# Kernel tuning notes

Hardware: AMD Instinct MI355X
Metric: run time of the kernel (lower is better)

Reference implementation:

```python
import jax, jax.numpy as jnp
import numpy as np

T, N, E, P, D, F = 24, 10000, 320000, 20000, 64, 32


def setup_inputs() -> dict:
    key = jax.random.key(0)
    ks = jax.random.split(key, 16)
    s = 0.05

    def nrm(k, shape):
        return jax.random.normal(k, shape, jnp.float32) * s

    return {
        "x": jax.random.normal(ks[0], (T, N, F + 2), jnp.float32),
        "dis": jax.random.uniform(ks[1], (N, N), dtype=jnp.float32),
        "src": jax.random.randint(ks[2], (E,), 0, N, jnp.int32),
        "dst": jax.random.randint(ks[3], (E,), 0, N, jnp.int32),
        "train_idx": jax.random.randint(ks[4], (2, P), 0, N, jnp.int32),
        "ru_W1": nrm(ks[5], (D + F, D)), "ru_b1": jnp.zeros((D,), jnp.float32),
        "ru_W2": nrm(ks[6], (D, D)), "ru_b2": jnp.zeros((D,), jnp.float32),
        "ru_W3": nrm(ks[7], (D, 2 * D)), "ru_b3": jnp.zeros((2 * D,), jnp.float32),
        "rh_W1": nrm(ks[8], (D + F, D)), "rh_b1": jnp.zeros((D,), jnp.float32),
        "rh_W2": nrm(ks[9], (D, D)), "rh_b2": jnp.zeros((D,), jnp.float32),
        "rh_W3": nrm(ks[10], (D, D)), "rh_b3": jnp.zeros((D,), jnp.float32),
        "pred_W": nrm(ks[11], (2 * D + 1, 1)), "pred_b": jnp.zeros((1,), jnp.float32),
    }


def reference(x, dis, src, dst, train_idx,
              ru_W1, ru_b1, ru_W2, ru_b2, ru_W3, ru_b3,
              rh_W1, rh_b1, rh_W2, rh_b2, rh_W3, rh_b3,
              pred_W, pred_b):
    # DGL GraphConv, norm='both': h <- D_in^{-1/2} A D_out^{-1/2} h W + b (deg clamped to >=1)
    ones = jnp.ones((E,), jnp.float32)
    out_norm = jax.lax.rsqrt(jnp.maximum(jax.ops.segment_sum(ones, src, num_segments=N), 1.0))
    in_norm = jax.lax.rsqrt(jnp.maximum(jax.ops.segment_sum(ones, dst, num_segments=N), 1.0))

    def gconv(h, W, b):
        m = (h * out_norm[:, None])[src]                              # gather [E, d]
        agg = jax.ops.segment_sum(m, dst, num_segments=N) * in_norm[:, None]
        return agg @ W + b

    def gnn(h, W1, b1, W2, b2, W3, b3):
        h = jax.nn.relu(gconv(h, W1, b1))
        h = jax.nn.relu(gconv(h, W2, b2))
        return gconv(h, W3, b3)

    feat = x[:, :, :-2]                                               # [T, N, F]

    def step(h, xt):
        ru = jax.nn.sigmoid(gnn(jnp.concatenate([h, xt], -1),
                                ru_W1, ru_b1, ru_W2, ru_b2, ru_W3, ru_b3))
        r, z = ru[:, :D], ru[:, D:]
        h_new = jnp.tanh(gnn(jnp.concatenate([h * r, xt], -1),
                             rh_W1, rh_b1, rh_W2, rh_b2, rh_W3, rh_b3))
        h = z * h + (1.0 - z) * h_new
        return h, h

    _, hs = jax.lax.scan(step, jnp.zeros((N, D), x.dtype), feat)      # [T, N, D]

    ori = hs[:, train_idx[0]]                                         # [T, P, D]
    dst_e = hs[:, train_idx[1]]                                       # [T, P, D]
    d = jnp.broadcast_to(dis[train_idx[0], train_idx[1]][None, :, None], (T, P, 1))
    flow = jnp.tanh(jnp.concatenate([ori, dst_e, d], -1) @ pred_W + pred_b)  # [T, P, 1]
    return flow[:, :, 0].T                                            # [P, T]
```

## Files before the change

### kernel.cpp

```cpp
#include <hip/hip_runtime.h>
#include <cstdint>
#include <cstddef>

#define T_ 24
#define N_ 10000
#define E_ 320000
#define P_ 20000
#define D_ 64
#define F_ 32
#define XS_ 34


__global__ void deg_kernel(const int* __restrict__ src, const int* __restrict__ dst,
                           int* __restrict__ deg_out, int* __restrict__ deg_in) {
  int e = blockIdx.x * blockDim.x + threadIdx.x;
  if (e < E_) {
    atomicAdd(&deg_out[src[e]], 1);
    atomicAdd(&deg_in[dst[e]], 1);
  }
}

__global__ void norm_kernel(const int* __restrict__ deg_in, const int* __restrict__ deg_out,
                            float* __restrict__ in_norm, float* __restrict__ out_norm) {
  int n = blockIdx.x * blockDim.x + threadIdx.x;
  if (n < N_) {
    in_norm[n]  = 1.0f / sqrtf(fmaxf((float)deg_in[n], 1.0f));
    out_norm[n] = 1.0f / sqrtf(fmaxf((float)deg_out[n], 1.0f));
  }
}

__global__ __launch_bounds__(1024) void scan_kernel(const int* __restrict__ deg,
                                                    int* __restrict__ row_ptr) {
  __shared__ int buf[1024];
  __shared__ int carry;
  int tid = threadIdx.x;
  if (tid == 0) { carry = 0; row_ptr[0] = 0; }
  __syncthreads();
  for (int base = 0; base < N_; base += 1024) {
    int i = base + tid;
    int v = (i < N_) ? deg[i] : 0;
    buf[tid] = v;
    __syncthreads();
    for (int off = 1; off < 1024; off <<= 1) {
      int tv = (tid >= off) ? buf[tid - off] : 0;
      __syncthreads();
      buf[tid] += tv;
      __syncthreads();
    }
    if (i < N_) row_ptr[i + 1] = carry + buf[tid];
    __syncthreads();
    if (tid == 0) carry += buf[1023];
    __syncthreads();
  }
}

__global__ void fill_kernel(const int* __restrict__ src, const int* __restrict__ dst,
                            const int* __restrict__ row_ptr, int* __restrict__ fill,
                            int* __restrict__ col) {
  int e = blockIdx.x * blockDim.x + threadIdx.x;
  if (e < E_) {
    int n = dst[e];
    int pos = row_ptr[n] + atomicAdd(&fill[n], 1);
    col[pos] = src[e];
  }
}

__global__ void dvec_kernel(const float* __restrict__ dis, const int* __restrict__ ti,
                            float* __restrict__ dvec) {
  int p = blockIdx.x * blockDim.x + threadIdx.x;
  if (p < P_) {
    int i0 = ti[p];
    int i1 = ti[P_ + p];
    dvec[p] = dis[(size_t)i0 * N_ + i1];
  }
}

__global__ __launch_bounds__(256) void pre_kernel(
    const float* __restrict__ hsrc, const float* __restrict__ xt,
    const float* __restrict__ out_norm, const float* __restrict__ W,
    float* __restrict__ tdst) {
  __shared__ float sIn[32][96];
  __shared__ float sW[96 * 64];
  const int tid = threadIdx.x;
  const int node0 = blockIdx.x * 32;

  {
    const float4* Wv = (const float4*)W;
    float4* sWv = (float4*)sW;
    for (int i = tid; i < 96 * 64 / 4; i += 256) sWv[i] = Wv[i];
  }
  for (int idx = tid; idx < 32 * 96; idx += 256) {
    int r = idx / 96, c = idx % 96;
    int n = node0 + r;
    float v = 0.0f;
    if (n < N_) {
      v = (c < 64) ? hsrc[(size_t)n * 64 + c] : xt[(size_t)n * XS_ + (c - 64)];
      v *= out_norm[n];
    }
    sIn[r][c] = v;
  }
  __syncthreads();

  const int o = tid & 63;
  const int q = tid >> 6;
  float acc[8];
#pragma unroll
  for (int j = 0; j < 8; ++j) acc[j] = 0.0f;
#pragma unroll 4
  for (int i = 0; i < 96; ++i) {
    float w = sW[i * 64 + o];
#pragma unroll
    for (int j = 0; j < 8; ++j) acc[j] += sIn[q * 8 + j][i] * w;
  }
#pragma unroll
  for (int j = 0; j < 8; ++j) {
    int n = node0 + q * 8 + j;
    if (n < N_) tdst[(size_t)n * 64 + o] = acc[j];
  }
}

template<int DOUT, int MODE>
__global__ __launch_bounds__(512) void gather_kernel(
    const float* __restrict__ t, const int* __restrict__ row_ptr,
    const int* __restrict__ col, const float* __restrict__ in_norm,
    const float* __restrict__ out_norm, const float* __restrict__ W,
    const float* __restrict__ bias, float* __restrict__ out,
    const float* __restrict__ hprev, float* __restrict__ hdst,
    const float* __restrict__ zsrc, float* __restrict__ zdst) {
  __shared__ float4 sAgg4[8][16];
  constexpr int WELEMS = (MODE == 1) ? 4 : (64 * DOUT);
  __shared__ float sW[WELEMS];

  const int tid = threadIdx.x;
  if constexpr (MODE != 1) {
    const float4* Wv = (const float4*)W;
    float4* sWv = (float4*)sW;
    for (int i = tid; i < WELEMS / 4; i += 512) sWv[i] = Wv[i];
  }

  const int wave = tid >> 6;
  const int lane = tid & 63;
  const int g = lane >> 4;
  const int sub = lane & 15;
  const int n = blockIdx.x * 8 + wave;

  float4 acc = make_float4(0.f, 0.f, 0.f, 0.f);
  if (n < N_) {
    int e0 = row_ptr[n], e1 = row_ptr[n + 1];
    int e = e0 + g;
    int snext = (e < e1) ? col[e] : 0;
    for (; e < e1; e += 4) {
      int s = snext;
      int en = e + 4;
      snext = (en < e1) ? col[en] : 0;
      float4 v = ((const float4*)(t + (size_t)s * 64))[sub];
      acc.x += v.x; acc.y += v.y; acc.z += v.z; acc.w += v.w;
    }
  }
#pragma unroll
  for (int off = 16; off < 64; off <<= 1) {
    acc.x += __shfl_xor(acc.x, off);
    acc.y += __shfl_xor(acc.y, off);
    acc.z += __shfl_xor(acc.z, off);
    acc.w += __shfl_xor(acc.w, off);
  }

  if (n < N_ && g == 0) {
    float inn = in_norm[n];
    float4 val;
    if constexpr (MODE == 0 || MODE == 1) {
      float on = out_norm[n];
      float4 b4 = ((const float4*)bias)[sub];
      val.x = on * fmaxf(inn * acc.x + b4.x, 0.0f);
      val.y = on * fmaxf(inn * acc.y + b4.y, 0.0f);
      val.z = on * fmaxf(inn * acc.z + b4.z, 0.0f);
      val.w = on * fmaxf(inn * acc.w + b4.w, 0.0f);
    } else {
      val.x = inn * acc.x; val.y = inn * acc.y;
      val.z = inn * acc.z; val.w = inn * acc.w;
    }
    if constexpr (MODE == 1) {
      ((float4*)(out + (size_t)n * 64))[sub] = val;
    } else {
      sAgg4[wave][sub] = val;
    }
  }
  if constexpr (MODE == 1) return;
  __syncthreads();

  if (n >= N_) return;
  const float* sAgg = (const float*)&sAgg4[wave][0];
  const int o = lane;

  if constexpr (MODE == 0) {
    float a = 0.0f;
#pragma unroll 8
    for (int i = 0; i < 64; ++i) a += sAgg[i] * sW[i * 64 + o];
    out[(size_t)n * 64 + o] = a;
  } else if constexpr (MODE == 2) {
    float a0 = bias[o], a1 = bias[o + 64];
#pragma unroll 8
    for (int i = 0; i < 64; ++i) {
      float ai = sAgg[i];
      a0 += ai * sW[i * 128 + o];
      a1 += ai * sW[i * 128 + o + 64];
    }
    float r = 1.0f / (1.0f + expf(-a0));
    float z = 1.0f / (1.0f + expf(-a1));
    hdst[(size_t)n * 64 + o] = r * hprev[(size_t)n * 64 + o];
    zdst[(size_t)n * 64 + o] = z;
  } else {
    float a = bias[o];
#pragma unroll 8
    for (int i = 0; i < 64; ++i) a += sAgg[i] * sW[i * 64 + o];
    float hn = tanhf(a);
    float zz = zsrc[(size_t)n * 64 + o];
    float hp = hprev[(size_t)n * 64 + o];
    hdst[(size_t)n * 64 + o] = zz * hp + (1.0f - zz) * hn;
  }
}

__global__ __launch_bounds__(256) void pred_kernel(
    const float* __restrict__ h, const int* __restrict__ ti,
    const float* __restrict__ dvec, const float* __restrict__ pW,
    const float* __restrict__ pb, float* __restrict__ out, int t) {
  const int tid = threadIdx.x;
  const int lane = tid & 63;
  const int wave = tid >> 6;
  const int g2 = lane >> 4;
  const int sub = lane & 15;
  const int p = blockIdx.x * 16 + wave * 4 + g2;
  if (p >= P_) return;

  int i0 = ti[p];
  int i1 = ti[P_ + p];
  float4 a0 = ((const float4*)(h + (size_t)i0 * 64))[sub];
  float4 w0 = ((const float4*)pW)[sub];
  float4 a1 = ((const float4*)(h + (size_t)i1 * 64))[sub];
  float4 w1 = ((const float4*)(pW + 64))[sub];
  float part = a0.x * w0.x + a0.y * w0.y + a0.z * w0.z + a0.w * w0.w
             + a1.x * w1.x + a1.y * w1.y + a1.z * w1.z + a1.w * w1.w;
#pragma unroll
  for (int off = 1; off < 16; off <<= 1) part += __shfl_xor(part, off);
  if (sub == 0) {
    float a = part + pb[0] + dvec[p] * pW[128];
    out[(size_t)p * T_ + t] = tanhf(a);
  }
}


extern "C" void kernel_launch(void* const* d_in, const int* in_sizes, int n_in,
                              void* d_out, int out_size, void* d_ws, size_t ws_size,
                              hipStream_t stream) {
  const float* x      = (const float*)d_in[0];
  const float* dis    = (const float*)d_in[1];
  const int*   src    = (const int*)d_in[2];
  const int*   dst    = (const int*)d_in[3];
  const int*   ti     = (const int*)d_in[4];
  const float* ru_W1  = (const float*)d_in[5];
  const float* ru_b1  = (const float*)d_in[6];
  const float* ru_W2  = (const float*)d_in[7];
  const float* ru_b2  = (const float*)d_in[8];
  const float* ru_W3  = (const float*)d_in[9];
  const float* ru_b3  = (const float*)d_in[10];
  const float* rh_W1  = (const float*)d_in[11];
  const float* rh_b1  = (const float*)d_in[12];
  const float* rh_W2  = (const float*)d_in[13];
  const float* rh_b2  = (const float*)d_in[14];
  const float* rh_W3  = (const float*)d_in[15];
  const float* rh_b3  = (const float*)d_in[16];
  const float* pred_W = (const float*)d_in[17];
  const float* pred_b = (const float*)d_in[18];
  float* out = (float*)d_out;

  char* w = (char*)d_ws;
  auto alloc = [&](size_t bytes) -> void* {
    void* p = (void*)w;
    w += (bytes + 255) & ~(size_t)255;
    return p;
  };
  int*   row_ptr  = (int*)alloc((N_ + 1) * sizeof(int));
  int*   colv     = (int*)alloc(E_ * sizeof(int));
  int*   deg_in   = (int*)alloc(N_ * sizeof(int));
  int*   deg_out  = (int*)alloc(N_ * sizeof(int));
  int*   fillc    = (int*)alloc(N_ * sizeof(int));
  float* in_norm  = (float*)alloc(N_ * sizeof(float));
  float* out_norm = (float*)alloc(N_ * sizeof(float));
  float* dvec     = (float*)alloc(P_ * sizeof(float));
  float* h        = (float*)alloc((size_t)N_ * D_ * sizeof(float));
  float* hr       = (float*)alloc((size_t)N_ * D_ * sizeof(float));
  float* z        = (float*)alloc((size_t)N_ * D_ * sizeof(float));
  float* tA       = (float*)alloc((size_t)N_ * D_ * sizeof(float));
  float* tB       = (float*)alloc((size_t)N_ * D_ * sizeof(float));

  hipMemsetAsync(deg_in, 0, N_ * sizeof(int), stream);
  hipMemsetAsync(deg_out, 0, N_ * sizeof(int), stream);
  hipMemsetAsync(fillc, 0, N_ * sizeof(int), stream);
  hipMemsetAsync(h, 0, (size_t)N_ * D_ * sizeof(float), stream);

  deg_kernel<<<(E_ + 255) / 256, 256, 0, stream>>>(src, dst, deg_out, deg_in);
  norm_kernel<<<(N_ + 255) / 256, 256, 0, stream>>>(deg_in, deg_out, in_norm, out_norm);
  scan_kernel<<<1, 1024, 0, stream>>>(deg_in, row_ptr);
  fill_kernel<<<(E_ + 255) / 256, 256, 0, stream>>>(src, dst, row_ptr, fillc, colv);
  dvec_kernel<<<(P_ + 255) / 256, 256, 0, stream>>>(dis, ti, dvec);

  const int GPRE = (N_ + 31) / 32;
  const int GGAT = (N_ + 7) / 8;
  const int GPRD = (P_ + 15) / 16;

  for (int t = 0; t < T_; ++t) {
    const float* xt = x + (size_t)t * N_ * XS_;
    pre_kernel<<<GPRE, 256, 0, stream>>>(h, xt, out_norm, ru_W1, tA);
    gather_kernel<64, 0><<<GGAT, 512, 0, stream>>>(
        tA, row_ptr, colv, in_norm, out_norm, ru_W2, ru_b1, tB,
        nullptr, nullptr, nullptr, nullptr);
    gather_kernel<64, 1><<<GGAT, 512, 0, stream>>>(
        tB, row_ptr, colv, in_norm, out_norm, nullptr, ru_b2, tA,
        nullptr, nullptr, nullptr, nullptr);
    gather_kernel<128, 2><<<GGAT, 512, 0, stream>>>(
        tA, row_ptr, colv, in_norm, out_norm, ru_W3, ru_b3, nullptr,
        h, hr, nullptr, z);
    pre_kernel<<<GPRE, 256, 0, stream>>>(hr, xt, out_norm, rh_W1, tA);
    gather_kernel<64, 0><<<GGAT, 512, 0, stream>>>(
        tA, row_ptr, colv, in_norm, out_norm, rh_W2, rh_b1, tB,
        nullptr, nullptr, nullptr, nullptr);
    gather_kernel<64, 1><<<GGAT, 512, 0, stream>>>(
        tB, row_ptr, colv, in_norm, out_norm, nullptr, rh_b2, tA,
        nullptr, nullptr, nullptr, nullptr);
    gather_kernel<64, 3><<<GGAT, 512, 0, stream>>>(
        tA, row_ptr, colv, in_norm, out_norm, rh_W3, rh_b3, nullptr,
        h, h, z, nullptr);
    pred_kernel<<<GPRD, 256, 0, stream>>>(h, ti, dvec, pred_W, pred_b, out, t);
  }
}
```

Measured before the change: 3.212 ms.

## Fuse all GRU timesteps into one persistent cooperative kernel with grid syncs

Replaces the 216 per-step kernel launches with a single cooperative persistent kernel that walks all timesteps and phases, separated by grid-wide barriers. The first-layer dense transform is folded into the preceding gather phase, so the hr buffer and the separate pre kernels go away. The prediction for step t-1 is run alongside the first phase of step t. The gather loop is also unrolled to keep two neighbour loads in flight. The aim is to remove launch gaps and intermediate memory round-trips, at the cost of 144 grid-wide barriers, a fixed grid size and possible load imbalance from contiguous node ranges.

```diff
diff --git a/kernel.cpp b/kernel.cpp
--- a/kernel.cpp
+++ b/kernel.cpp
@@ -1,4 +1,5 @@
 #include <hip/hip_runtime.h>
+#include <hip/hip_cooperative_groups.h>
 #include <cstdint>
 #include <cstddef>
 
@@ -9,6 +10,8 @@
 #define D_ 64
 #define F_ 32
 #define XS_ 34
+
+namespace cg = cooperative_groups;
 
 
 __global__ void deg_kernel(const int* __restrict__ src, const int* __restrict__ dst,
@@ -75,87 +78,50 @@
   }
 }
 
-__global__ __launch_bounds__(256) void pre_kernel(
-    const float* __restrict__ hsrc, const float* __restrict__ xt,
-    const float* __restrict__ out_norm, const float* __restrict__ W,
-    float* __restrict__ tdst) {
-  __shared__ float sIn[32][96];
-  __shared__ float sW[96 * 64];
-  const int tid = threadIdx.x;
-  const int node0 = blockIdx.x * 32;
-
-  {
-    const float4* Wv = (const float4*)W;
-    float4* sWv = (float4*)sW;
-    for (int i = tid; i < 96 * 64 / 4; i += 256) sWv[i] = Wv[i];
-  }
-  for (int idx = tid; idx < 32 * 96; idx += 256) {
-    int r = idx / 96, c = idx % 96;
-    int n = node0 + r;
-    float v = 0.0f;
-    if (n < N_) {
-      v = (c < 64) ? hsrc[(size_t)n * 64 + c] : xt[(size_t)n * XS_ + (c - 64)];
-      v *= out_norm[n];
-    }
-    sIn[r][c] = v;
-  }
-  __syncthreads();
-
-  const int o = tid & 63;
-  const int q = tid >> 6;
-  float acc[8];
-#pragma unroll
-  for (int j = 0; j < 8; ++j) acc[j] = 0.0f;
-#pragma unroll 4
-  for (int i = 0; i < 96; ++i) {
-    float w = sW[i * 64 + o];
-#pragma unroll
-    for (int j = 0; j < 8; ++j) acc[j] += sIn[q * 8 + j][i] * w;
-  }
-#pragma unroll
-  for (int j = 0; j < 8; ++j) {
-    int n = node0 + q * 8 + j;
-    if (n < N_) tdst[(size_t)n * 64 + o] = acc[j];
-  }
-}
-
-template<int DOUT, int MODE>
-__global__ __launch_bounds__(512) void gather_kernel(
-    const float* __restrict__ t, const int* __restrict__ row_ptr,
-    const int* __restrict__ col, const float* __restrict__ in_norm,
-    const float* __restrict__ out_norm, const float* __restrict__ W,
-    const float* __restrict__ bias, float* __restrict__ out,
-    const float* __restrict__ hprev, float* __restrict__ hdst,
-    const float* __restrict__ zsrc, float* __restrict__ zdst) {
-  __shared__ float4 sAgg4[8][16];
-  constexpr int WELEMS = (MODE == 1) ? 4 : (64 * DOUT);
-  __shared__ float sW[WELEMS];
-
-  const int tid = threadIdx.x;
-  if constexpr (MODE != 1) {
-    const float4* Wv = (const float4*)W;
-    float4* sWv = (float4*)sW;
-    for (int i = tid; i < WELEMS / 4; i += 512) sWv[i] = Wv[i];
-  }
-
-  const int wave = tid >> 6;
-  const int lane = tid & 63;
-  const int g = lane >> 4;
-  const int sub = lane & 15;
-  const int n = blockIdx.x * 8 + wave;
-
+
+struct Args {
+  const float* x;
+  const int* row_ptr;
+  const int* col;
+  const float* in_norm;
+  const float* out_norm;
+  const float* ruW1; const float* ruB1;
+  const float* ruW2; const float* ruB2;
+  const float* ruW3; const float* ruB3;
+  const float* rhW1; const float* rhB1;
+  const float* rhW2; const float* rhB2;
+  const float* rhW3; const float* rhB3;
+  const float* pW; const float* pb;
+  const int* ti; const float* dvec;
+  float* h; float* z; float* tA; float* tB;
+  float* out;
+};
+
+__device__ __forceinline__ void stageW(const float* __restrict__ W, int n4,
+                                       float4* __restrict__ sdst, int tid) {
+  const float4* Wv = (const float4*)W;
+  for (int i = tid; i < n4; i += 512) sdst[i] = Wv[i];
+}
+
+__device__ __forceinline__ float4 gatherNode(const float* __restrict__ tsrc,
+                                             const int* __restrict__ rp,
+                                             const int* __restrict__ col,
+                                             int n, int g, int sub) {
+  int e0 = rp[n], e1 = rp[n + 1];
   float4 acc = make_float4(0.f, 0.f, 0.f, 0.f);
-  if (n < N_) {
-    int e0 = row_ptr[n], e1 = row_ptr[n + 1];
-    int e = e0 + g;
-    int snext = (e < e1) ? col[e] : 0;
-    for (; e < e1; e += 4) {
-      int s = snext;
-      int en = e + 4;
-      snext = (en < e1) ? col[en] : 0;
-      float4 v = ((const float4*)(t + (size_t)s * 64))[sub];
-      acc.x += v.x; acc.y += v.y; acc.z += v.z; acc.w += v.w;
-    }
+  int e = e0 + g;
+  int c0 = (e < e1) ? col[e] : 0;
+  int c1 = (e + 4 < e1) ? col[e + 4] : 0;
+  while (e < e1) {
+    bool has1 = (e + 4 < e1);
+    float4 v0 = ((const float4*)(tsrc + (size_t)c0 * 64))[sub];
+    float4 v1 = make_float4(0.f, 0.f, 0.f, 0.f);
+    if (has1) v1 = ((const float4*)(tsrc + (size_t)c1 * 64))[sub];
+    int c2 = (e + 8 < e1) ? col[e + 8] : 0;
+    int c3 = (e + 12 < e1) ? col[e + 12] : 0;
+    acc.x += v0.x; acc.y += v0.y; acc.z += v0.z; acc.w += v0.w;
+    acc.x += v1.x; acc.y += v1.y; acc.z += v1.z; acc.w += v1.w;
+    c0 = c2; c1 = c3; e += 8;
   }
 #pragma unroll
   for (int off = 16; off < 64; off <<= 1) {
@@ -164,88 +130,203 @@
     acc.z += __shfl_xor(acc.z, off);
     acc.w += __shfl_xor(acc.w, off);
   }
-
-  if (n < N_ && g == 0) {
-    float inn = in_norm[n];
-    float4 val;
-    if constexpr (MODE == 0 || MODE == 1) {
-      float on = out_norm[n];
-      float4 b4 = ((const float4*)bias)[sub];
-      val.x = on * fmaxf(inn * acc.x + b4.x, 0.0f);
-      val.y = on * fmaxf(inn * acc.y + b4.y, 0.0f);
-      val.z = on * fmaxf(inn * acc.z + b4.z, 0.0f);
-      val.w = on * fmaxf(inn * acc.w + b4.w, 0.0f);
+  return acc;
+}
+
+__device__ __forceinline__ void predPhase(const Args& A, int t, int wgid, int WT,
+                                          int g, int sub) {
+  for (int q = wgid; q * 4 < P_; q += WT) {
+    int p = q * 4 + g;
+    bool valid = (p < P_);
+    int i0 = valid ? A.ti[p] : 0;
+    int i1 = valid ? A.ti[P_ + p] : 0;
+    float4 a0 = ((const float4*)(A.h + (size_t)i0 * 64))[sub];
+    float4 w0 = ((const float4*)A.pW)[sub];
+    float4 a1 = ((const float4*)(A.h + (size_t)i1 * 64))[sub];
+    float4 w1 = ((const float4*)(A.pW + 64))[sub];
+    float part = a0.x * w0.x + a0.y * w0.y + a0.z * w0.z + a0.w * w0.w
+               + a1.x * w1.x + a1.y * w1.y + a1.z * w1.z + a1.w * w1.w;
+#pragma unroll
+    for (int off = 1; off < 16; off <<= 1) part += __shfl_xor(part, off);
+    if (valid && sub == 0) {
+      float a = part + A.pb[0] + A.dvec[p] * A.pW[128];
+      A.out[(size_t)p * T_ + t] = tanhf(a);
+    }
+  }
+}
+
+template<int MODE>
+__device__ __forceinline__ void runPhase(
+    const Args& A, const float* __restrict__ tsrc, float* __restrict__ tdst,
+    const float* __restrict__ W, const float* __restrict__ bias,
+    const float* __restrict__ Wpre, const float* __restrict__ xside,
+    float4* sWv, float4* sWpreV, float (*sRow)[96], float4 (*sAgg4)[16],
+    int tid, int nodeBase, int nodeEnd, bool doPre) {
+  const int wave = tid >> 6;
+  const int lane = tid & 63;
+  const int g = lane >> 4;
+  const int sub = lane & 15;
+
+  if (MODE == 0) stageW(W, 64 * 64 / 4, sWv, tid);
+  if (MODE == 2) { stageW(W, 64 * 128 / 4, sWv, tid); stageW(Wpre, 96 * 64 / 4, sWpreV, tid); }
+  if (MODE == 3) { stageW(W, 64 * 64 / 4, sWv, tid); if (doPre) stageW(Wpre, 96 * 64 / 4, sWpreV, tid); }
+  if (MODE != 1) __syncthreads();
+
+  const float* sW = (const float*)sWv;
+  const float* sWpre = (const float*)sWpreV;
+
+  float4 b4 = make_float4(0.f, 0.f, 0.f, 0.f);
+  float b0 = 0.f, b1 = 0.f;
+  if (MODE == 0 || MODE == 1) {
+    b4 = ((const float4*)bias)[sub];
+  } else if (MODE == 2) {
+    b0 = bias[lane]; b1 = bias[64 + lane];
+  } else {
+    b0 = bias[lane];
+  }
+
+  for (int n = nodeBase + wave; n < nodeEnd; n += 8) {
+    float4 acc = gatherNode(tsrc, A.row_ptr, A.col, n, g, sub);
+    float inn = A.in_norm[n];
+    float on = A.out_norm[n];
+
+    if (MODE == 0 || MODE == 1) {
+      if (g == 0) {
+        float4 val;
+        val.x = on * fmaxf(inn * acc.x + b4.x, 0.0f);
+        val.y = on * fmaxf(inn * acc.y + b4.y, 0.0f);
+        val.z = on * fmaxf(inn * acc.z + b4.z, 0.0f);
+        val.w = on * fmaxf(inn * acc.w + b4.w, 0.0f);
+        if (MODE == 1) ((float4*)(tdst + (size_t)n * 64))[sub] = val;
+        else           sAgg4[wave][sub] = val;
+      }
+      if (MODE == 0) {
+        const float* sAgg = (const float*)&sAgg4[wave][0];
+        float a = 0.0f;
+#pragma unroll 8
+        for (int i = 0; i < 64; ++i) a += sAgg[i] * sW[i * 64 + lane];
+        tdst[(size_t)n * 64 + lane] = a;
+      }
+    } else if (MODE == 2) {
+      if (g == 0) {
+        float4 val;
+        val.x = inn * acc.x; val.y = inn * acc.y;
+        val.z = inn * acc.z; val.w = inn * acc.w;
+        sAgg4[wave][sub] = val;
+      }
+      const float* sAgg = (const float*)&sAgg4[wave][0];
+      float a0 = b0, a1 = b1;
+#pragma unroll 8
+      for (int i = 0; i < 64; ++i) {
+        float s = sAgg[i];
+        a0 += s * sW[i * 128 + lane];
+        a1 += s * sW[i * 128 + 64 + lane];
+      }
+      float r = 1.0f / (1.0f + expf(-a0));
+      float zz = 1.0f / (1.0f + expf(-a1));
+      A.z[(size_t)n * 64 + lane] = zz;
+      float hrv = r * A.h[(size_t)n * 64 + lane];
+      sRow[wave][lane] = on * hrv;
+      if (lane < 32) sRow[wave][64 + lane] = on * xside[(size_t)n * XS_ + lane];
+      float a = 0.0f;
+#pragma unroll 8
+      for (int i = 0; i < 96; ++i) a += sRow[wave][i] * sWpre[i * 64 + lane];
+      tdst[(size_t)n * 64 + lane] = a;
     } else {
-      val.x = inn * acc.x; val.y = inn * acc.y;
-      val.z = inn * acc.z; val.w = inn * acc.w;
+      if (g == 0) {
+        float4 val;
+        val.x = inn * acc.x; val.y = inn * acc.y;
+        val.z = inn * acc.z; val.w = inn * acc.w;
+        sAgg4[wave][sub] = val;
+      }
+      const float* sAgg = (const float*)&sAgg4[wave][0];
+      float a = b0;
+#pragma unroll 8
+      for (int i = 0; i < 64; ++i) a += sAgg[i] * sW[i * 64 + lane];
+      float hn = tanhf(a);
+      float zz = A.z[(size_t)n * 64 + lane];
+      float hp = A.h[(size_t)n * 64 + lane];
+      float hnew = zz * hp + (1.0f - zz) * hn;
+      A.h[(size_t)n * 64 + lane] = hnew;
+      if (doPre) {
+        sRow[wave][lane] = on * hnew;
+        if (lane < 32) sRow[wave][64 + lane] = on * xside[(size_t)n * XS_ + lane];
+        float ap = 0.0f;
+#pragma unroll 8
+        for (int i = 0; i < 96; ++i) ap += sRow[wave][i] * sWpre[i * 64 + lane];
+        tdst[(size_t)n * 64 + lane] = ap;
+      }
     }
-    if constexpr (MODE == 1) {
-      ((float4*)(out + (size_t)n * 64))[sub] = val;
-    } else {
-      sAgg4[wave][sub] = val;
+  }
+}
+
+__global__ __launch_bounds__(512, 4) void mega_kernel(Args A) {
+  cg::grid_group grid = cg::this_grid();
+
+  __shared__ float4 sWv[2048];
+  __shared__ float4 sWpreV[1536];
+  __shared__ float sRow[8][96];
+  __shared__ float4 sAgg4[8][16];
+
+  const int tid = threadIdx.x;
+  const int wave = tid >> 6;
+  const int lane = tid & 63;
+  const int g = lane >> 4;
+  const int sub = lane & 15;
+  const int nblk = gridDim.x;
+  const int NPB = (N_ + nblk - 1) / nblk;
+  const int nodeBase = blockIdx.x * NPB;
+  int nodeEnd = nodeBase + NPB;
+  if (nodeEnd > N_) nodeEnd = N_;
+  const int wgid = blockIdx.x * 8 + wave;
+  const int WT = nblk * 8;
+
+  stageW(A.ruW1, 96 * 64 / 4, sWpreV, tid);
+  __syncthreads();
+  {
+    const float* sWpre = (const float*)sWpreV;
+    for (int n = nodeBase + wave; n < nodeEnd; n += 8) {
+      float on = A.out_norm[n];
+      if (lane < 32) sRow[wave][64 + lane] = on * A.x[(size_t)n * XS_ + lane];
+      float a = 0.0f;
+#pragma unroll 8
+      for (int i = 64; i < 96; ++i) a += sRow[wave][i] * sWpre[i * 64 + lane];
+      A.tA[(size_t)n * 64 + lane] = a;
     }
   }
-  if constexpr (MODE == 1) return;
-  __syncthreads();
-
-  if (n >= N_) return;
-  const float* sAgg = (const float*)&sAgg4[wave][0];
-  const int o = lane;
-
-  if constexpr (MODE == 0) {
-    float a = 0.0f;
-#pragma unroll 8
-    for (int i = 0; i < 64; ++i) a += sAgg[i] * sW[i * 64 + o];
-    out[(size_t)n * 64 + o] = a;
-  } else if constexpr (MODE == 2) {
-    float a0 = bias[o], a1 = bias[o + 64];
-#pragma unroll 8
-    for (int i = 0; i < 64; ++i) {
-      float ai = sAgg[i];
-      a0 += ai * sW[i * 128 + o];
-      a1 += ai * sW[i * 128 + o + 64];
-    }
-    float r = 1.0f / (1.0f + expf(-a0));
-    float z = 1.0f / (1.0f + expf(-a1));
-    hdst[(size_t)n * 64 + o] = r * hprev[(size_t)n * 64 + o];
-    zdst[(size_t)n * 64 + o] = z;
-  } else {
-    float a = bias[o];
-#pragma unroll 8
-    for (int i = 0; i < 64; ++i) a += sAgg[i] * sW[i * 64 + o];
-    float hn = tanhf(a);
-    float zz = zsrc[(size_t)n * 64 + o];
-    float hp = hprev[(size_t)n * 64 + o];
-    hdst[(size_t)n * 64 + o] = zz * hp + (1.0f - zz) * hn;
-  }
-}
-
-__global__ __launch_bounds__(256) void pred_kernel(
-    const float* __restrict__ h, const int* __restrict__ ti,
-    const float* __restrict__ dvec, const float* __restrict__ pW,
-    const float* __restrict__ pb, float* __restrict__ out, int t) {
-  const int tid = threadIdx.x;
-  const int lane = tid & 63;
-  const int wave = tid >> 6;
-  const int g2 = lane >> 4;
-  const int sub = lane & 15;
-  const int p = blockIdx.x * 16 + wave * 4 + g2;
-  if (p >= P_) return;
-
-  int i0 = ti[p];
-  int i1 = ti[P_ + p];
-  float4 a0 = ((const float4*)(h + (size_t)i0 * 64))[sub];
-  float4 w0 = ((const float4*)pW)[sub];
-  float4 a1 = ((const float4*)(h + (size_t)i1 * 64))[sub];
-  float4 w1 = ((const float4*)(pW + 64))[sub];
-  float part = a0.x * w0.x + a0.y * w0.y + a0.z * w0.z + a0.w * w0.w
-             + a1.x * w1.x + a1.y * w1.y + a1.z * w1.z + a1.w * w1.w;
-#pragma unroll
-  for (int off = 1; off < 16; off <<= 1) part += __shfl_xor(part, off);
-  if (sub == 0) {
-    float a = part + pb[0] + dvec[p] * pW[128];
-    out[(size_t)p * T_ + t] = tanhf(a);
-  }
+  grid.sync();
+
+  for (int t = 0; t < T_; ++t) {
+    const float* xt  = A.x + (size_t)t * N_ * XS_;
+    const float* xt1 = A.x + (size_t)(t + 1) * N_ * XS_;
+
+    runPhase<0>(A, A.tA, A.tB, A.ruW2, A.ruB1, nullptr, nullptr,
+                sWv, sWpreV, sRow, sAgg4, tid, nodeBase, nodeEnd, false);
+    if (t > 0) predPhase(A, t - 1, wgid, WT, g, sub);
+    grid.sync();
+
+    runPhase<1>(A, A.tB, A.tA, nullptr, A.ruB2, nullptr, nullptr,
+                sWv, sWpreV, sRow, sAgg4, tid, nodeBase, nodeEnd, false);
+    grid.sync();
+
+    runPhase<2>(A, A.tA, A.tB, A.ruW3, A.ruB3, A.rhW1, xt,
+                sWv, sWpreV, sRow, sAgg4, tid, nodeBase, nodeEnd, false);
+    grid.sync();
+
+    runPhase<0>(A, A.tB, A.tA, A.rhW2, A.rhB1, nullptr, nullptr,
+                sWv, sWpreV, sRow, sAgg4, tid, nodeBase, nodeEnd, false);
+    grid.sync();
+
+    runPhase<1>(A, A.tA, A.tB, nullptr, A.rhB2, nullptr, nullptr,
+                sWv, sWpreV, sRow, sAgg4, tid, nodeBase, nodeEnd, false);
+    grid.sync();
+
+    runPhase<3>(A, A.tB, A.tA, A.rhW3, A.rhB3, A.ruW1, xt1,
+                sWv, sWpreV, sRow, sAgg4, tid, nodeBase, nodeEnd, t < T_ - 1);
+    grid.sync();
+  }
+
+  predPhase(A, T_ - 1, wgid, WT, g, sub);
 }
 
 
@@ -288,7 +369,6 @@
   float* out_norm = (float*)alloc(N_ * sizeof(float));
   float* dvec     = (float*)alloc(P_ * sizeof(float));
   float* h        = (float*)alloc((size_t)N_ * D_ * sizeof(float));
-  float* hr       = (float*)alloc((size_t)N_ * D_ * sizeof(float));
   float* z        = (float*)alloc((size_t)N_ * D_ * sizeof(float));
   float* tA       = (float*)alloc((size_t)N_ * D_ * sizeof(float));
   float* tB       = (float*)alloc((size_t)N_ * D_ * sizeof(float));
@@ -304,32 +384,23 @@
   fill_kernel<<<(E_ + 255) / 256, 256, 0, stream>>>(src, dst, row_ptr, fillc, colv);
   dvec_kernel<<<(P_ + 255) / 256, 256, 0, stream>>>(dis, ti, dvec);
 
-  const int GPRE = (N_ + 31) / 32;
-  const int GGAT = (N_ + 7) / 8;
-  const int GPRD = (P_ + 15) / 16;
-
-  for (int t = 0; t < T_; ++t) {
-    const float* xt = x + (size_t)t * N_ * XS_;
-    pre_kernel<<<GPRE, 256, 0, stream>>>(h, xt, out_norm, ru_W1, tA);
-    gather_kernel<64, 0><<<GGAT, 512, 0, stream>>>(
-        tA, row_ptr, colv, in_norm, out_norm, ru_W2, ru_b1, tB,
-        nullptr, nullptr, nullptr, nullptr);
-    gather_kernel<64, 1><<<GGAT, 512, 0, stream>>>(
-        tB, row_ptr, colv, in_norm, out_norm, nullptr, ru_b2, tA,
-        nullptr, nullptr, nullptr, nullptr);
-    gather_kernel<128, 2><<<GGAT, 512, 0, stream>>>(
-        tA, row_ptr, colv, in_norm, out_norm, ru_W3, ru_b3, nullptr,
-        h, hr, nullptr, z);
-    pre_kernel<<<GPRE, 256, 0, stream>>>(hr, xt, out_norm, rh_W1, tA);
-    gather_kernel<64, 0><<<GGAT, 512, 0, stream>>>(
-        tA, row_ptr, colv, in_norm, out_norm, rh_W2, rh_b1, tB,
-        nullptr, nullptr, nullptr, nullptr);
-    gather_kernel<64, 1><<<GGAT, 512, 0, stream>>>(
-        tB, row_ptr, colv, in_norm, out_norm, nullptr, rh_b2, tA,
-        nullptr, nullptr, nullptr, nullptr);
-    gather_kernel<64, 3><<<GGAT, 512, 0, stream>>>(
-        tA, row_ptr, colv, in_norm, out_norm, rh_W3, rh_b3, nullptr,
-        h, h, z, nullptr);
-    pred_kernel<<<GPRD, 256, 0, stream>>>(h, ti, dvec, pred_W, pred_b, out, t);
-  }
-}
+  Args a;
+  a.x = x; a.row_ptr = row_ptr; a.col = colv;
+  a.in_norm = in_norm; a.out_norm = out_norm;
+  a.ruW1 = ru_W1; a.ruB1 = ru_b1; a.ruW2 = ru_W2; a.ruB2 = ru_b2;
+  a.ruW3 = ru_W3; a.ruB3 = ru_b3;
+  a.rhW1 = rh_W1; a.rhB1 = rh_b1; a.rhW2 = rh_W2; a.rhB2 = rh_b2;
+  a.rhW3 = rh_W3; a.rhB3 = rh_b3;
+  a.pW = pred_W; a.pb = pred_b; a.ti = ti; a.dvec = dvec;
+  a.h = h; a.z = z; a.tA = tA; a.tB = tB; a.out = out;
+
+  int maxb = 0;
+  hipOccupancyMaxActiveBlocksPerMultiprocessor(&maxb, mega_kernel, 512, 0);
+  if (maxb < 1) maxb = 1;
+  int bpc = (maxb < 2) ? maxb : 2;
+  int nblk = 256 * bpc;
+
+  void* params[] = { (void*)&a };
+  hipLaunchCooperativeKernel((const void*)mega_kernel, dim3(nblk), dim3(512),
+                             params, 0, stream);
+}
```

Result: slower. 7.146 ms (+122.5%).
